# Kernel optimization log

Measured on AMD Instinct MI355X. Metric: run time of the kernel, lower is better.

## Reference

```python
import jax, jax.numpy as jnp
import numpy as np


def setup_inputs() -> dict:
    key = jax.random.key(0)
    ks = jax.random.split(key, 16)
    H, F, W, Hh, C = 8, 256, 96, 96, 64
    inp = {
        "X": jax.random.normal(ks[0], (F, W, Hh), jnp.float32),
        "WQ_task": jax.random.uniform(ks[1], (H, F, 1, 1), jnp.float32),
        "BQ_task": jax.random.uniform(ks[2], (H, F, 1, 1), jnp.float32),
        "WK_task": jax.random.uniform(ks[3], (F, 1, 1), jnp.float32),
        "BK_task": jax.random.uniform(ks[4], (F, 1, 1), jnp.float32),
        "WV_task": jax.random.uniform(ks[5], (C, 1, 1), jnp.float32),
        "BV_task": jax.random.uniform(ks[6], (C, 1, 1), jnp.float32),
        "WQ_t_minus_1": jax.random.uniform(ks[7], (H, F, 1, 1), jnp.float32),
        "WQ_x": jax.random.uniform(ks[8], (1, F, 1, 1), jnp.float32),
        "BQ": jax.random.uniform(ks[9], (H, F, 1, 1), jnp.float32),
        "WK_x": jax.random.uniform(ks[10], (F, 1, 1), jnp.float32),
        "BK": jax.random.uniform(ks[11], (F, 1, 1), jnp.float32),
        "prev_Q": jax.random.normal(ks[12], (H, F, W, Hh), jnp.float32),
        "Vconv_w": jax.random.normal(ks[13], (C, F, 3, 3), jnp.float32) * 0.02,
        "Vconv_b": jnp.zeros((C,), jnp.float32),
    }
    return inp


def reference(X, WQ_task, BQ_task, WK_task, BK_task, WV_task, BV_task,
              WQ_t_minus_1, WQ_x, BQ, WK_x, BK, prev_Q, Vconv_w, Vconv_b):
    F, W, Hh = X.shape
    C = Vconv_w.shape[0]
    rX = X[None]  # (1, F, W, Hh)

    # Q: (n_heads, F, W, Hh); K: (F, W, Hh)
    Q = WQ_task * (WQ_t_minus_1 * prev_Q + WQ_x * rX + BQ) + BQ_task
    K = WK_task * (WK_x * X + BK) + BK_task

    # Original: similarity = sum over [head, feature] of Q[n,f,w,h] * K[f,v,u]
    # (K is broadcast over heads) == dot(Q.sum(heads), K) over features.
    Qs = Q.sum(axis=0)  # (F, W, Hh)
    sim = jnp.einsum('fwh,fvu->whvu', Qs, K).reshape(W, Hh, W * Hh)
    attn = jax.nn.softmax(sim, axis=-1)  # softmax over flattened key positions

    # V: 3x3 same conv F -> C, then task affine
    V = jax.lax.conv_general_dilated(
        rX, Vconv_w, window_strides=(1, 1), padding='SAME',
        dimension_numbers=('NCHW', 'OIHW', 'NCHW'))
    V = (WV_task * (V[0] + Vconv_b[:, None, None]) + BV_task).reshape(C, W * Hh)

    # out[c, w, h] = sum_k attn[w, h, k] * V[c, k]
    out = jnp.einsum('whk,ck->cwh', attn, V)
    return out
```

## Files before the change

### kernel.cpp

```cpp
#include <hip/hip_runtime.h>
#include <hip/hip_fp16.h>

#define S 9216
#define F 256
#define W 96
#define HH 96
#define C 64
#define NH 8
#define KSPLIT 8
#define KV_PER_SPLIT (S / KSPLIT)
#define KTILE 64
#define NKT (KV_PER_SPLIT / KTILE)

typedef _Float16 half8 __attribute__((ext_vector_type(8)));
typedef float floatx4 __attribute__((ext_vector_type(4)));


__global__ __launch_bounds__(256) void rowmean_kernel(
    const float* __restrict__ prevQ, const float* __restrict__ Xg,
    float* __restrict__ pqmean, float* __restrict__ xmean) {
  int row = blockIdx.x;
  const float4* src = (const float4*)((row < 2048) ? (prevQ + (size_t)row * S)
                                                   : (Xg + (size_t)(row - 2048) * S));
  float s = 0.f;
  #pragma unroll
  for (int j = 0; j < 9; j++) {
    float4 v = src[j * 256 + threadIdx.x];
    s += v.x + v.y + v.z + v.w;
  }
  __shared__ float red[256];
  red[threadIdx.x] = s;
  __syncthreads();
  for (int off = 128; off > 0; off >>= 1) {
    if ((int)threadIdx.x < off) red[threadIdx.x] += red[threadIdx.x + off];
    __syncthreads();
  }
  if (threadIdx.x == 0) {
    float m = red[0] * (1.f / (float)S);
    if (row < 2048) pqmean[row] = m; else xmean[row - 2048] = m;
  }
}

__global__ __launch_bounds__(256) void coef_kernel(
    const float* __restrict__ WQ_task, const float* __restrict__ BQ_task,
    const float* __restrict__ WK_task, const float* __restrict__ BK_task,
    const float* __restrict__ WQ_tm1, const float* __restrict__ WQ_x,
    const float* __restrict__ BQ, const float* __restrict__ WK_x,
    const float* __restrict__ BK, const float* __restrict__ pqmean,
    const float* __restrict__ xmean,
    float* __restrict__ qscale, float* __restrict__ c1, float* __restrict__ c0,
    float* __restrict__ kw, float* __restrict__ kb,
    float* __restrict__ qbar, float* __restrict__ kbar) {
  int f = threadIdx.x;
  float sumW = 0.f, sc0 = 0.f, qb = 0.f;
  for (int n = 0; n < NH; n++) {
    float wq = WQ_task[n * F + f];
    float qs = wq * WQ_tm1[n * F + f];
    qscale[f * NH + n] = qs;
    sumW += wq;
    sc0 += wq * BQ[n * F + f] + BQ_task[n * F + f];
    qb += qs * pqmean[n * F + f];
  }
  float c1v = WQ_x[f] * sumW;
  c1[f] = c1v; c0[f] = sc0;
  float kwv = WK_task[f] * WK_x[f];
  float kbv = WK_task[f] * BK[f] + BK_task[f];
  kw[f] = kwv; kb[f] = kbv;
  qbar[f] = qb + c1v * xmean[f] + sc0;
  kbar[f] = kwv * xmean[f] + kbv;
}

__global__ __launch_bounds__(256) void prep_kernel(
    const float* __restrict__ Xg, const float* __restrict__ prevQ,
    const float* __restrict__ qscale, const float* __restrict__ c1,
    const float* __restrict__ c0, const float* __restrict__ kw,
    const float* __restrict__ kb, const float* __restrict__ qbar,
    const float* __restrict__ kbar,
    _Float16* __restrict__ Qf, _Float16* __restrict__ Kf,
    float* __restrict__ rowK) {
  __shared__ float qt[32][33];
  __shared__ float kt[32][33];
  __shared__ float rk[8][32];
  int tx = threadIdx.x & 31, ty = threadIdx.x >> 5;
  int s0 = blockIdx.x * 32, f0 = blockIdx.y * 32;
  int s = s0 + tx;
  float rkacc = 0.f;
  for (int fi = ty; fi < 32; fi += 8) {
    int f = f0 + fi;
    float x = Xg[(size_t)f * S + s];
    float q = c1[f] * x + c0[f];
    #pragma unroll
    for (int n = 0; n < NH; n++)
      q += qscale[f * NH + n] * prevQ[((size_t)n * F + f) * S + s];
    q -= qbar[f];
    float k = kw[f] * x + kb[f] - kbar[f];
    qt[fi][tx] = q;
    kt[fi][tx] = k;
    rkacc += qbar[f] * k;
  }
  rk[ty][tx] = rkacc;
  __syncthreads();
  {
    int t = threadIdx.x;
    int isK = t >> 7;
    int tt = t & 127;
    int s_sub = tt >> 2, lw = tt & 3;
    half8 h;
    #pragma unroll
    for (int jj = 0; jj < 8; jj++) {
      float v = isK ? kt[lw * 8 + jj][s_sub] : qt[lw * 8 + jj][s_sub];
      h[jj] = (_Float16)v;
    }
    size_t fi = (size_t)((s0 + s_sub) >> 4) * 8 + (f0 >> 5);
    int lane = (s_sub & 15) + 16 * lw;
    half8* dst = (half8*)(isK ? Kf : Qf);
    dst[fi * 64 + lane] = h;
  }
  if (ty == 0) {
    float t = 0.f;
    #pragma unroll
    for (int i = 0; i < 8; i++) t += rk[i][tx];
    atomicAdd(&rowK[s], t);
  }
}

__global__ __launch_bounds__(256) void conv_kernel(
    const float* __restrict__ Xg, const float* __restrict__ Wc,
    const float* __restrict__ bias, const float* __restrict__ WV_task,
    const float* __restrict__ BV_task, _Float16* __restrict__ Vf) {
  __shared__ float wlds[4 * 2304];
  int c0 = blockIdx.y * 4;
  for (int i = threadIdx.x; i < 4 * 2304; i += 256)
    wlds[i] = Wc[(size_t)c0 * 2304 + i];
  __syncthreads();
  int p = blockIdx.x * 256 + threadIdx.x;
  int w = p / HH, h = p % HH;
  float acc0 = 0.f, acc1 = 0.f, acc2 = 0.f, acc3 = 0.f;
  for (int f = 0; f < F; f++) {
    const float* xp = Xg + (size_t)f * S;
    float xv[9];
    #pragma unroll
    for (int ky = 0; ky < 3; ky++) {
      int ww = w + ky - 1;
      #pragma unroll
      for (int kx = 0; kx < 3; kx++) {
        int hh = h + kx - 1;
        xv[ky * 3 + kx] = (ww >= 0 && ww < W && hh >= 0 && hh < HH)
                              ? xp[ww * HH + hh] : 0.f;
      }
    }
    const float* wl = wlds + f * 9;
    #pragma unroll
    for (int t = 0; t < 9; t++) {
      float x = xv[t];
      acc0 += x * wl[t];
      acc1 += x * wl[2304 + t];
      acc2 += x * wl[2 * 2304 + t];
      acc3 += x * wl[3 * 2304 + t];
    }
  }
  float accs[4] = {acc0, acc1, acc2, acc3};
  int k = p;
  #pragma unroll
  for (int cc = 0; cc < 4; cc++) {
    int c = c0 + cc;
    float v = WV_task[c] * (accs[cc] + bias[c]) + BV_task[c];
    size_t idx = (((size_t)(k >> 5) * 4 + (c >> 4)) * 64 +
                  ((c & 15) + 16 * ((k & 31) >> 3))) * 8 + (k & 7);
    Vf[idx] = (_Float16)v;
  }
}

__global__ __launch_bounds__(256, 2) void flash_kernel(
    const _Float16* __restrict__ Qf, const _Float16* __restrict__ Kf,
    const _Float16* __restrict__ Vf, const float* __restrict__ rowK,
    float* __restrict__ out_part, float* __restrict__ m_part,
    float* __restrict__ l_part) {
  int qt = blockIdx.x, sp = blockIdx.y;
  int wave = threadIdx.x >> 6, lane = threadIdx.x & 63;
  int lr = lane & 15, lhi = lane >> 4;
  __shared__ __align__(16) _Float16 kvbuf[2560 * 8];
  __shared__ __align__(16) _Float16 plds[4][16][72];
  half8* ldsv = (half8*)kvbuf;

  half8 qfrag[2][8];
  {
    const half8* qb = (const half8*)Qf;
    #pragma unroll
    for (int qs = 0; qs < 2; qs++) {
      size_t t16 = (size_t)(qt * 8 + wave * 2 + qs) * 8;
      #pragma unroll
      for (int ch = 0; ch < 8; ch++) qfrag[qs][ch] = qb[(t16 + ch) * 64 + lane];
    }
  }

  floatx4 oacc[2][4] = {};
  float m_run[2][4], l_run[2][4];
  #pragma unroll
  for (int qs = 0; qs < 2; qs++)
    #pragma unroll
    for (int j = 0; j < 4; j++) { m_run[qs][j] = -1e30f; l_run[qs][j] = 0.f; }

  for (int kt = 0; kt < NKT; kt++) {
    int k0 = sp * KV_PER_SPLIT + kt * KTILE;
    const half8* ksrc = (const half8*)Kf + (size_t)(k0 >> 4) * 512;
    const half8* vsrc = (const half8*)Vf + (size_t)(k0 >> 5) * 256;
    __syncthreads();
    #pragma unroll
    for (int j = 0; j < 10; j++) {
      int idx = j * 256 + (int)threadIdx.x;
      const half8* src = (idx < 2048) ? (ksrc + idx) : (vsrc + (idx - 2048));
      ldsv[idx] = *src;
    }
    __syncthreads();

    float rk4[4];
    #pragma unroll
    for (int ks = 0; ks < 4; ks++) rk4[ks] = rowK[k0 + ks * 16 + lr];

    floatx4 sacc[2][4] = {};
    #pragma unroll
    for (int ch = 0; ch < 8; ch++) {
      #pragma unroll
      for (int ks = 0; ks < 4; ks++) {
        half8 kf = ldsv[(ks * 8 + ch) * 64 + lane];
        sacc[0][ks] = __builtin_amdgcn_mfma_f32_16x16x32_f16(qfrag[0][ch], kf,
                                                             sacc[0][ks], 0, 0, 0);
        sacc[1][ks] = __builtin_amdgcn_mfma_f32_16x16x32_f16(qfrag[1][ch], kf,
                                                             sacc[1][ks], 0, 0, 0);
      }
    }

    #pragma unroll
    for (int qs = 0; qs < 2; qs++) {
      float tmax[4];
      #pragma unroll
      for (int j = 0; j < 4; j++) tmax[j] = -1e30f;
      #pragma unroll
      for (int ks = 0; ks < 4; ks++) {
        #pragma unroll
        for (int j = 0; j < 4; j++) {
          sacc[qs][ks][j] += rk4[ks];
          tmax[j] = fmaxf(tmax[j], sacc[qs][ks][j]);
        }
      }
      #pragma unroll
      for (int off = 1; off < 16; off <<= 1)
        #pragma unroll
        for (int j = 0; j < 4; j++)
          tmax[j] = fmaxf(tmax[j], __shfl_xor(tmax[j], off, 64));

      float ef[4], rsum[4];
      #pragma unroll
      for (int j = 0; j < 4; j++) {
        float mn = fmaxf(m_run[qs][j], tmax[j]);
        ef[j] = __expf(m_run[qs][j] - mn);
        m_run[qs][j] = mn;
        rsum[j] = 0.f;
      }
      #pragma unroll
      for (int ks = 0; ks < 4; ks++) {
        #pragma unroll
        for (int j = 0; j < 4; j++) {
          float p = __expf(sacc[qs][ks][j] - m_run[qs][j]);
          rsum[j] += p;
          plds[wave][lhi * 4 + j][ks * 16 + lr] = (_Float16)p;
        }
      }
      #pragma unroll
      for (int off = 1; off < 16; off <<= 1)
        #pragma unroll
        for (int j = 0; j < 4; j++) rsum[j] += __shfl_xor(rsum[j], off, 64);
      #pragma unroll
      for (int j = 0; j < 4; j++)
        l_run[qs][j] = l_run[qs][j] * ef[j] + rsum[j];
      #pragma unroll
      for (int cs = 0; cs < 4; cs++)
        #pragma unroll
        for (int j = 0; j < 4; j++) oacc[qs][cs][j] *= ef[j];

      #pragma unroll
      for (int kc = 0; kc < 2; kc++) {
        half8 pfrag = *(const half8*)(&plds[wave][lr][kc * 32 + lhi * 8]);
        #pragma unroll
        for (int cs = 0; cs < 4; cs++) {
          half8 vfrag = ldsv[2048 + (kc * 4 + cs) * 64 + lane];
          oacc[qs][cs] = __builtin_amdgcn_mfma_f32_16x16x32_f16(pfrag, vfrag,
                                                                oacc[qs][cs], 0, 0, 0);
        }
      }
    }
  }

  #pragma unroll
  for (int qs = 0; qs < 2; qs++) {
    size_t base = (size_t)sp * S + qt * 128 + wave * 32 + qs * 16;
    #pragma unroll
    for (int cs = 0; cs < 4; cs++)
      #pragma unroll
      for (int j = 0; j < 4; j++)
        out_part[(base + lhi * 4 + j) * C + cs * 16 + lr] = oacc[qs][cs][j];
    if (lr == 0) {
      #pragma unroll
      for (int j = 0; j < 4; j++) {
        m_part[base + lhi * 4 + j] = m_run[qs][j];
        l_part[base + lhi * 4 + j] = l_run[qs][j];
      }
    }
  }
}

__global__ __launch_bounds__(256) void combine_kernel(
    const float* __restrict__ out_part, const float* __restrict__ m_part,
    const float* __restrict__ l_part, float* __restrict__ out) {
  int q = blockIdx.x * 4 + (threadIdx.x >> 6);
  int c = threadIdx.x & 63;
  float m = -1e30f;
  #pragma unroll
  for (int i = 0; i < KSPLIT; i++) m = fmaxf(m, m_part[(size_t)i * S + q]);
  float l = 0.f, acc = 0.f;
  #pragma unroll
  for (int i = 0; i < KSPLIT; i++) {
    float wgt = __expf(m_part[(size_t)i * S + q] - m);
    l += wgt * l_part[(size_t)i * S + q];
    acc += wgt * out_part[((size_t)i * S + q) * C + c];
  }
  out[(size_t)c * S + q] = acc / l;
}

extern "C" void kernel_launch(void* const* d_in, const int* in_sizes, int n_in,
                              void* d_out, int out_size, void* d_ws,
                              size_t ws_size, hipStream_t stream) {
  const float* Xg      = (const float*)d_in[0];
  const float* WQ_task = (const float*)d_in[1];
  const float* BQ_task = (const float*)d_in[2];
  const float* WK_task = (const float*)d_in[3];
  const float* BK_task = (const float*)d_in[4];
  const float* WV_task = (const float*)d_in[5];
  const float* BV_task = (const float*)d_in[6];
  const float* WQ_tm1  = (const float*)d_in[7];
  const float* WQ_x    = (const float*)d_in[8];
  const float* BQ      = (const float*)d_in[9];
  const float* WK_x    = (const float*)d_in[10];
  const float* BK      = (const float*)d_in[11];
  const float* prevQ   = (const float*)d_in[12];
  const float* Wc      = (const float*)d_in[13];
  const float* bias    = (const float*)d_in[14];
  float* out = (float*)d_out;

  char* ws = (char*)d_ws;
  size_t off = 0;
  auto alloc = [&](size_t bytes) {
    void* p = ws + off;
    off += (bytes + 255) & ~(size_t)255;
    return p;
  };
  _Float16* Qf   = (_Float16*)alloc((size_t)S * F * 2);
  _Float16* Kf   = (_Float16*)alloc((size_t)S * F * 2);
  _Float16* Vf   = (_Float16*)alloc((size_t)C * S * 2);
  float* rowK    = (float*)alloc((size_t)S * 4);
  float* pqmean  = (float*)alloc(2048 * 4);
  float* xmean   = (float*)alloc(256 * 4);
  float* qscale  = (float*)alloc(256 * 8 * 4);
  float* c1      = (float*)alloc(256 * 4);
  float* c0      = (float*)alloc(256 * 4);
  float* kw      = (float*)alloc(256 * 4);
  float* kb      = (float*)alloc(256 * 4);
  float* qbar    = (float*)alloc(256 * 4);
  float* kbar    = (float*)alloc(256 * 4);
  float* out_part = (float*)alloc((size_t)KSPLIT * S * C * 4);
  float* m_part   = (float*)alloc((size_t)KSPLIT * S * 4);
  float* l_part   = (float*)alloc((size_t)KSPLIT * S * 4);

  hipMemsetAsync(rowK, 0, (size_t)S * 4, stream);

  rowmean_kernel<<<2304, 256, 0, stream>>>(prevQ, Xg, pqmean, xmean);
  coef_kernel<<<1, 256, 0, stream>>>(WQ_task, BQ_task, WK_task, BK_task,
                                     WQ_tm1, WQ_x, BQ, WK_x, BK, pqmean, xmean,
                                     qscale, c1, c0, kw, kb, qbar, kbar);
  prep_kernel<<<dim3(S / 32, F / 32), 256, 0, stream>>>(
      Xg, prevQ, qscale, c1, c0, kw, kb, qbar, kbar, Qf, Kf, rowK);
  conv_kernel<<<dim3(S / 256, C / 4), 256, 0, stream>>>(Xg, Wc, bias, WV_task,
                                                        BV_task, Vf);
  flash_kernel<<<dim3(S / 128, KSPLIT), 256, 0, stream>>>(
      Qf, Kf, Vf, rowK, out_part, m_part, l_part);
  combine_kernel<<<S / 4, 256, 0, stream>>>(out_part, m_part, l_part, out);
}
```

Baseline: 535.5 us.

## Double-buffer K/V tiles in flash kernel, raise split count, store partials in fp16

The flash attention kernel now prefetches the next K/V tile into registers while computing on the current one and writes it to a second LDS buffer. This removes one barrier per iteration and hides global load latency behind the MFMA work. The KV tile shrinks to 32, the split count rises to 16, occupancy is hinted to 3 blocks per CU, and the partial outputs are stored as fp16 to cut combine traffic. The costs are more per-iteration overhead from smaller tiles, twice as many partials to combine, and some precision loss in the fp16 partials.

New measurement: 472.9 us. 11.7% less time.

```diff
diff --git a/kernel.cpp b/kernel.cpp
--- a/kernel.cpp
+++ b/kernel.cpp
@@ -7,10 +7,11 @@
 #define HH 96
 #define C 64
 #define NH 8
-#define KSPLIT 8
+#define KSPLIT 16
 #define KV_PER_SPLIT (S / KSPLIT)
-#define KTILE 64
+#define KTILE 32
 #define NKT (KV_PER_SPLIT / KTILE)
+#define TILE_H8 1280
 
 typedef _Float16 half8 __attribute__((ext_vector_type(8)));
 typedef float floatx4 __attribute__((ext_vector_type(4)));
@@ -171,27 +172,25 @@
   }
 }
 
-__global__ __launch_bounds__(256, 2) void flash_kernel(
+__global__ __launch_bounds__(256, 3) void flash_kernel(
     const _Float16* __restrict__ Qf, const _Float16* __restrict__ Kf,
     const _Float16* __restrict__ Vf, const float* __restrict__ rowK,
-    float* __restrict__ out_part, float* __restrict__ m_part,
+    _Float16* __restrict__ out_part, float* __restrict__ m_part,
     float* __restrict__ l_part) {
   int qt = blockIdx.x, sp = blockIdx.y;
   int wave = threadIdx.x >> 6, lane = threadIdx.x & 63;
+  int tid = threadIdx.x;
   int lr = lane & 15, lhi = lane >> 4;
-  __shared__ __align__(16) _Float16 kvbuf[2560 * 8];
-  __shared__ __align__(16) _Float16 plds[4][16][72];
-  half8* ldsv = (half8*)kvbuf;
+  __shared__ __align__(16) half8 kv[2][TILE_H8];
+  __shared__ __align__(16) _Float16 plds[4][16][40];
 
   half8 qfrag[2][8];
-  {
-    const half8* qb = (const half8*)Qf;
-    #pragma unroll
-    for (int qs = 0; qs < 2; qs++) {
-      size_t t16 = (size_t)(qt * 8 + wave * 2 + qs) * 8;
-      #pragma unroll
-      for (int ch = 0; ch < 8; ch++) qfrag[qs][ch] = qb[(t16 + ch) * 64 + lane];
-    }
+  #pragma unroll
+  for (int qs = 0; qs < 2; qs++) {
+    size_t t16 = (size_t)(qt * 8 + wave * 2 + qs) * 8;
+    #pragma unroll
+    for (int ch = 0; ch < 8; ch++)
+      qfrag[qs][ch] = ((const half8*)Qf)[(t16 + ch) * 64 + lane];
   }
 
   floatx4 oacc[2][4] = {};
@@ -201,29 +200,43 @@
     #pragma unroll
     for (int j = 0; j < 4; j++) { m_run[qs][j] = -1e30f; l_run[qs][j] = 0.f; }
 
+  {
+    int k0 = sp * KV_PER_SPLIT;
+    const half8* ks = (const half8*)Kf + (size_t)(k0 >> 4) * 512;
+    const half8* vs = (const half8*)Vf + (size_t)(k0 >> 5) * 256;
+    #pragma unroll
+    for (int u = 0; u < 5; u++) {
+      int idx = u * 256 + tid;
+      kv[0][idx] = (idx < 1024) ? ks[idx] : vs[idx - 1024];
+    }
+  }
+
+  int cur = 0;
   for (int kt = 0; kt < NKT; kt++) {
     int k0 = sp * KV_PER_SPLIT + kt * KTILE;
-    const half8* ksrc = (const half8*)Kf + (size_t)(k0 >> 4) * 512;
-    const half8* vsrc = (const half8*)Vf + (size_t)(k0 >> 5) * 256;
+    half8 stg[5];
+    if (kt + 1 < NKT) {
+      const half8* ks = (const half8*)Kf + (size_t)((k0 + KTILE) >> 4) * 512;
+      const half8* vs = (const half8*)Vf + (size_t)((k0 + KTILE) >> 5) * 256;
+      #pragma unroll
+      for (int u = 0; u < 5; u++) {
+        int idx = u * 256 + tid;
+        stg[u] = (idx < 1024) ? ks[idx] : vs[idx - 1024];
+      }
+    }
+    __builtin_amdgcn_sched_barrier(0);
     __syncthreads();
-    #pragma unroll
-    for (int j = 0; j < 10; j++) {
-      int idx = j * 256 + (int)threadIdx.x;
-      const half8* src = (idx < 2048) ? (ksrc + idx) : (vsrc + (idx - 2048));
-      ldsv[idx] = *src;
-    }
-    __syncthreads();
-
-    float rk4[4];
-    #pragma unroll
-    for (int ks = 0; ks < 4; ks++) rk4[ks] = rowK[k0 + ks * 16 + lr];
-
-    floatx4 sacc[2][4] = {};
+
+    float rk4[2];
+    #pragma unroll
+    for (int ks = 0; ks < 2; ks++) rk4[ks] = rowK[k0 + ks * 16 + lr];
+
+    floatx4 sacc[2][2] = {};
     #pragma unroll
     for (int ch = 0; ch < 8; ch++) {
       #pragma unroll
-      for (int ks = 0; ks < 4; ks++) {
-        half8 kf = ldsv[(ks * 8 + ch) * 64 + lane];
+      for (int ks = 0; ks < 2; ks++) {
+        half8 kf = kv[cur][(ks * 8 + ch) * 64 + lane];
         sacc[0][ks] = __builtin_amdgcn_mfma_f32_16x16x32_f16(qfrag[0][ch], kf,
                                                              sacc[0][ks], 0, 0, 0);
         sacc[1][ks] = __builtin_amdgcn_mfma_f32_16x16x32_f16(qfrag[1][ch], kf,
@@ -237,7 +250,7 @@
       #pragma unroll
       for (int j = 0; j < 4; j++) tmax[j] = -1e30f;
       #pragma unroll
-      for (int ks = 0; ks < 4; ks++) {
+      for (int ks = 0; ks < 2; ks++) {
         #pragma unroll
         for (int j = 0; j < 4; j++) {
           sacc[qs][ks][j] += rk4[ks];
@@ -259,7 +272,7 @@
         rsum[j] = 0.f;
       }
       #pragma unroll
-      for (int ks = 0; ks < 4; ks++) {
+      for (int ks = 0; ks < 2; ks++) {
         #pragma unroll
         for (int j = 0; j < 4; j++) {
           float p = __expf(sacc[qs][ks][j] - m_run[qs][j]);
@@ -279,17 +292,20 @@
         #pragma unroll
         for (int j = 0; j < 4; j++) oacc[qs][cs][j] *= ef[j];
 
-      #pragma unroll
-      for (int kc = 0; kc < 2; kc++) {
-        half8 pfrag = *(const half8*)(&plds[wave][lr][kc * 32 + lhi * 8]);
-        #pragma unroll
-        for (int cs = 0; cs < 4; cs++) {
-          half8 vfrag = ldsv[2048 + (kc * 4 + cs) * 64 + lane];
-          oacc[qs][cs] = __builtin_amdgcn_mfma_f32_16x16x32_f16(pfrag, vfrag,
-                                                                oacc[qs][cs], 0, 0, 0);
-        }
-      }
-    }
+      half8 pfrag = *(const half8*)(&plds[wave][lr][lhi * 8]);
+      #pragma unroll
+      for (int cs = 0; cs < 4; cs++) {
+        half8 vfrag = kv[cur][1024 + cs * 64 + lane];
+        oacc[qs][cs] = __builtin_amdgcn_mfma_f32_16x16x32_f16(pfrag, vfrag,
+                                                              oacc[qs][cs], 0, 0, 0);
+      }
+    }
+
+    if (kt + 1 < NKT) {
+      #pragma unroll
+      for (int u = 0; u < 5; u++) kv[cur ^ 1][u * 256 + tid] = stg[u];
+    }
+    cur ^= 1;
   }
 
   #pragma unroll
@@ -299,7 +315,8 @@
     for (int cs = 0; cs < 4; cs++)
       #pragma unroll
       for (int j = 0; j < 4; j++)
-        out_part[(base + lhi * 4 + j) * C + cs * 16 + lr] = oacc[qs][cs][j];
+        out_part[(base + lhi * 4 + j) * C + cs * 16 + lr] =
+            (_Float16)oacc[qs][cs][j];
     if (lr == 0) {
       #pragma unroll
       for (int j = 0; j < 4; j++) {
@@ -311,7 +328,7 @@
 }
 
 __global__ __launch_bounds__(256) void combine_kernel(
-    const float* __restrict__ out_part, const float* __restrict__ m_part,
+    const _Float16* __restrict__ out_part, const float* __restrict__ m_part,
     const float* __restrict__ l_part, float* __restrict__ out) {
   int q = blockIdx.x * 4 + (threadIdx.x >> 6);
   int c = threadIdx.x & 63;
@@ -323,7 +340,7 @@
   for (int i = 0; i < KSPLIT; i++) {
     float wgt = __expf(m_part[(size_t)i * S + q] - m);
     l += wgt * l_part[(size_t)i * S + q];
-    acc += wgt * out_part[((size_t)i * S + q) * C + c];
+    acc += wgt * (float)out_part[((size_t)i * S + q) * C + c];
   }
   out[(size_t)c * S + q] = acc / l;
 }
@@ -368,7 +385,7 @@
   float* kb      = (float*)alloc(256 * 4);
   float* qbar    = (float*)alloc(256 * 4);
   float* kbar    = (float*)alloc(256 * 4);
-  float* out_part = (float*)alloc((size_t)KSPLIT * S * C * 4);
+  _Float16* out_part = (_Float16*)alloc((size_t)KSPLIT * S * C * 2);
   float* m_part   = (float*)alloc((size_t)KSPLIT * S * 4);
   float* l_part   = (float*)alloc((size_t)KSPLIT * S * 4);
 
```
